# Optimization experiments

Hardware: AMD Instinct MI355X
Metric: run time of the kernel (lower is better)

## Reference

```python
import jax, jax.numpy as jnp
import numpy as np

B, N, D_IN, D_H, D_OUT = 32, 512, 512, 512, 512


def _xavier(key, fan_in, fan_out):
    bound = np.sqrt(6.0 / (fan_in + fan_out))
    return jax.random.uniform(key, (fan_in, fan_out), jnp.float32, -bound, bound)


def setup_inputs() -> dict:
    key = jax.random.key(0)
    ks = jax.random.split(key, 8)
    batch_graph = jax.random.normal(ks[0], (B, N, D_IN), jnp.float32)
    adj = jax.random.uniform(ks[1], (B, N, N), jnp.float32)  # per-graph adjacency blocks
    W0 = _xavier(ks[2], D_IN, D_H)
    b0 = jnp.zeros((D_H,), jnp.float32)
    W1 = _xavier(ks[3], D_H, D_H)
    b1 = jnp.zeros((D_H,), jnp.float32)
    W2 = _xavier(ks[4], D_H, D_OUT)
    b2 = jnp.zeros((D_OUT,), jnp.float32)
    return {"batch_graph": batch_graph, "adj": adj,
            "W0": W0, "b0": b0, "W1": W1, "b1": b1, "W2": W2, "b2": b2}


def _gcn_layer(h, adj, W, b):
    # GraphConvolution: adj @ (h @ W) + b, batched per graph.
    # Equivalent to big_adj @ (big_graph @ W) since big_adj is block-diagonal.
    support = jnp.einsum('bnd,de->bne', h, W)
    return jnp.einsum('bnm,bme->bne', adj, support) + b


def reference(batch_graph, adj, W0, b0, W1, b1, W2, b2):
    # dropout is identity at inference time
    h = jax.nn.relu(_gcn_layer(batch_graph, adj, W0, b0))
    h = jax.nn.relu(_gcn_layer(h, adj, W1, b1))
    h = _gcn_layer(h, adj, W2, b2)  # no activation on final layer
    return h  # [B, N, D_OUT] == torch.stack(big_graph.split(N))
```

## Files before the change

kernel.cpp:

```cpp
#include <hip/hip_runtime.h>
#include <stdint.h>

typedef __bf16 bf16x8 __attribute__((ext_vector_type(8)));
typedef float f32x4 __attribute__((ext_vector_type(4)));
typedef unsigned short u16x4 __attribute__((ext_vector_type(4)));

static __device__ __forceinline__ unsigned short f2bf(float f) {
    union { float f; unsigned u; } v; v.f = f;
    unsigned r = (v.u + 0x7FFFu + ((v.u >> 16) & 1u)) >> 16;
    return (unsigned short)r;
}

__global__ void prep_kernel(const float* __restrict__ X,
                            const float* __restrict__ adj,
                            const float* __restrict__ W0,
                            const float* __restrict__ W1,
                            const float* __restrict__ W2,
                            unsigned short* __restrict__ bufH,
                            unsigned short* __restrict__ adjB,
                            unsigned short* __restrict__ Wt) {
    const int bid = blockIdx.x;
    const int t = threadIdx.x;
    if (bid < 16384) {
        const float* src = (bid < 8192) ? X : adj;
        unsigned short* dst = (bid < 8192) ? bufH : adjB;
        const int i = (bid & 8191) * 256 + t;
        f32x4 v = ((const f32x4*)src)[i];
        u16x4 o;
        o.x = f2bf(v.x); o.y = f2bf(v.y); o.z = f2bf(v.z); o.w = f2bf(v.w);
        ((u16x4*)dst)[i] = o;
    } else {
        const int wb = bid - 16384;
        const int z = wb >> 8;
        const int tile = wb & 255;
        const float* W = (z == 0) ? W0 : (z == 1) ? W1 : W2;
        unsigned short* out = Wt + (size_t)z * (512 * 512);
        __shared__ float tileS[32][33];
        const int bx = (tile & 15) * 32, by = (tile >> 4) * 32;
        const int tx = t & 31, ty = t >> 5;
        #pragma unroll
        for (int r = 0; r < 32; r += 8)
            tileS[ty + r][tx] = W[(size_t)(by + ty + r) * 512 + (bx + tx)];
        __syncthreads();
        #pragma unroll
        for (int r = 0; r < 32; r += 8)
            out[(size_t)(bx + ty + r) * 512 + (by + tx)] = f2bf(tileS[tx][ty + r]);
    }
}

template<int LDA, int LDB, int LDO, bool BIAS, bool RELU, typename OT>
__global__ __launch_bounds__(256, 2)
void gemm_abT_ct(const unsigned short* __restrict__ A,
                 const unsigned short* __restrict__ B,
                 OT* __restrict__ out, const float* __restrict__ bias,
                 long batchA, long batchB, long batchO) {
    __shared__ unsigned short As[2][128 * 64];
    __shared__ unsigned short Bs[2][128 * 64];

    const int tid  = threadIdx.x;
    const int lane = tid & 63;
    const int wave = tid >> 6;
    const int quad = lane >> 4;
    const int l16  = lane & 15;
    const int wm   = wave & 1;
    const int wn   = wave >> 1;

    const int m0 = blockIdx.x * 128;
    const int n0 = blockIdx.y * 128;
    A   += (size_t)blockIdx.z * batchA;
    B   += (size_t)blockIdx.z * batchB;
    out += (size_t)blockIdx.z * batchO;

    const int trow8 = tid >> 3;
    const int tpos8 = (tid & 7) ^ (trow8 & 7);
    const unsigned short* aG = A + (size_t)(m0 + trow8) * LDA + tpos8 * 8;
    const unsigned short* bG = B + (size_t)(n0 + trow8) * LDB + tpos8 * 8;

    f32x4 acc[4][4];
    #pragma unroll
    for (int i = 0; i < 4; ++i)
        #pragma unroll
        for (int j = 0; j < 4; ++j) {
            f32x4 z = {0.f, 0.f, 0.f, 0.f};
            acc[i][j] = z;
        }

#define STAGE(buf, ko)                                                         \
    do {                                                                       \
        char* aL = (char*)As[buf] + tid * 16;                                  \
        char* bL = (char*)Bs[buf] + tid * 16;                                  \
        _Pragma("unroll")                                                      \
        for (int r = 0; r < 4; ++r)                                            \
            __builtin_amdgcn_global_load_lds(                                  \
                (__attribute__((address_space(1))) void*)(uintptr_t)(aG + (size_t)(r * 32) * LDA + (ko)), \
                (__attribute__((address_space(3))) void*)(aL + r * 4096), 16, 0, 0); \
        _Pragma("unroll")                                                      \
        for (int r = 0; r < 4; ++r)                                            \
            __builtin_amdgcn_global_load_lds(                                  \
                (__attribute__((address_space(1))) void*)(uintptr_t)(bG + (size_t)(r * 32) * LDB + (ko)), \
                (__attribute__((address_space(3))) void*)(bL + r * 4096), 16, 0, 0); \
    } while (0)

#define COMPUTE(buf)                                                           \
    do {                                                                       \
        _Pragma("unroll")                                                      \
        for (int ks = 0; ks < 2; ++ks) {                                       \
            bf16x8 af[4], bfr[4];                                              \
            _Pragma("unroll")                                                  \
            for (int i = 0; i < 4; ++i) {                                      \
                const int row = wm * 64 + i * 16 + l16;                        \
                const int idx = row * 8 + ((ks * 4 + quad) ^ (row & 7));       \
                af[i] = *(const bf16x8*)((const char*)As[buf] + idx * 16);     \
            }                                                                  \
            _Pragma("unroll")                                                  \
            for (int j = 0; j < 4; ++j) {                                      \
                const int row = wn * 64 + j * 16 + l16;                        \
                const int idx = row * 8 + ((ks * 4 + quad) ^ (row & 7));       \
                bfr[j] = *(const bf16x8*)((const char*)Bs[buf] + idx * 16);    \
            }                                                                  \
            _Pragma("unroll")                                                  \
            for (int i = 0; i < 4; ++i)                                        \
                _Pragma("unroll")                                              \
                for (int j = 0; j < 4; ++j)                                    \
                    acc[i][j] = __builtin_amdgcn_mfma_f32_16x16x32_bf16(af[i], bfr[j], acc[i][j], 0, 0, 0); \
        }                                                                      \
    } while (0)

    STAGE(0, 0);
    __syncthreads();

    #pragma unroll 1
    for (int kp = 0; kp < 4; ++kp) {
        STAGE(1, kp * 128 + 64);
        COMPUTE(0);
        __syncthreads();
        if (kp < 3) STAGE(0, kp * 128 + 128);
        COMPUTE(1);
        __syncthreads();
    }
#undef STAGE
#undef COMPUTE

    #pragma unroll
    for (int i = 0; i < 4; ++i) {
        const int mb = m0 + wm * 64 + i * 16 + quad * 4;
        f32x4 bb = {0.f, 0.f, 0.f, 0.f};
        if constexpr (BIAS) bb = *(const f32x4*)(bias + mb);
        #pragma unroll
        for (int j = 0; j < 4; ++j) {
            const int n = n0 + wn * 64 + j * 16 + l16;
            f32x4 v = acc[i][j];
            if constexpr (BIAS) v += bb;
            if constexpr (RELU) {
                v.x = v.x > 0.f ? v.x : 0.f;
                v.y = v.y > 0.f ? v.y : 0.f;
                v.z = v.z > 0.f ? v.z : 0.f;
                v.w = v.w > 0.f ? v.w : 0.f;
            }
            if constexpr (sizeof(OT) == 4) {
                *(f32x4*)((float*)out + (size_t)n * LDO + mb) = v;
            } else {
                u16x4 o;
                o.x = f2bf(v.x); o.y = f2bf(v.y); o.z = f2bf(v.z); o.w = f2bf(v.w);
                *(u16x4*)((unsigned short*)out + (size_t)n * LDO + mb) = o;
            }
        }
    }
}

extern "C" void kernel_launch(void* const* d_in, const int* in_sizes, int n_in,
                              void* d_out, int out_size, void* d_ws, size_t ws_size,
                              hipStream_t stream) {
    (void)in_sizes; (void)n_in; (void)out_size; (void)ws_size;
    const float* X   = (const float*)d_in[0];
    const float* adj = (const float*)d_in[1];
    const float* W0  = (const float*)d_in[2];
    const float* b0  = (const float*)d_in[3];
    const float* W1  = (const float*)d_in[4];
    const float* b1  = (const float*)d_in[5];
    const float* W2  = (const float*)d_in[6];
    const float* b2  = (const float*)d_in[7];
    float* out = (float*)d_out;

    char* ws = (char*)d_ws;
    const size_t SZ = 16777216;
    unsigned short* adjB = (unsigned short*)(ws);
    unsigned short* bufH = (unsigned short*)(ws + SZ);
    unsigned short* tmpT = (unsigned short*)(ws + 2 * SZ);
    unsigned short* Wt   = (unsigned short*)(ws + 3 * SZ);
    const unsigned short* W0t = Wt;
    const unsigned short* W1t = Wt + 262144;
    const unsigned short* W2t = Wt + 2 * 262144;

    prep_kernel<<<16384 + 768, 256, 0, stream>>>(X, adj, W0, W1, W2, bufH, adjB, Wt);

    const long BATCH = 512L * 512L;

    gemm_abT_ct<512, 512, 16384, false, false, unsigned short>
        <<<dim3(128, 4, 1), 256, 0, stream>>>(bufH, W0t, tmpT, nullptr, 0, 0, 0);
    gemm_abT_ct<16384, 512, 512, true, true, unsigned short>
        <<<dim3(4, 4, 32), 256, 0, stream>>>(tmpT, adjB, bufH, b0, 512, BATCH, BATCH);
    gemm_abT_ct<512, 512, 16384, false, false, unsigned short>
        <<<dim3(128, 4, 1), 256, 0, stream>>>(bufH, W1t, tmpT, nullptr, 0, 0, 0);
    gemm_abT_ct<16384, 512, 512, true, true, unsigned short>
        <<<dim3(4, 4, 32), 256, 0, stream>>>(tmpT, adjB, bufH, b1, 512, BATCH, BATCH);
    gemm_abT_ct<512, 512, 16384, false, false, unsigned short>
        <<<dim3(128, 4, 1), 256, 0, stream>>>(bufH, W2t, tmpT, nullptr, 0, 0, 0);
    gemm_abT_ct<16384, 512, 512, true, false, float>
        <<<dim3(4, 4, 32), 256, 0, stream>>>(tmpT, adjB, out, b2, 512, BATCH, BATCH);
}
```

Baseline: 229.2 us.

## Fuse six GEMM launches into one persistent kernel with grid barriers

Replaces the six separate GEMM launches with a single persistent 512-block kernel that runs each stage and separates them with atomic-counter grid-wide barriers. The counters are reset inside the prep kernel. The GEMM main loop is also reworked to keep two K-stages in flight, using explicit vmcnt waits, raw s_barrier and s_setprio around the MFMA blocks. The aim is to remove launch gaps and tail effects between dependent stages. In exchange it depends on all 512 blocks being co-resident (2 per CU) to avoid deadlock, and it adds spin-wait overhead.

```diff
diff --git a/kernel.cpp b/kernel.cpp
--- a/kernel.cpp
+++ b/kernel.cpp
@@ -18,10 +18,12 @@
                             const float* __restrict__ W2,
                             unsigned short* __restrict__ bufH,
                             unsigned short* __restrict__ adjB,
-                            unsigned short* __restrict__ Wt) {
+                            unsigned short* __restrict__ Wt,
+                            unsigned* __restrict__ syncc) {
     const int bid = blockIdx.x;
     const int t = threadIdx.x;
     if (bid < 16384) {
+        if (bid == 0 && t < 8) syncc[t] = 0u;
         const float* src = (bid < 8192) ? X : adj;
         unsigned short* dst = (bid < 8192) ? bufH : adjB;
         const int i = (bid & 8191) * 256 + t;
@@ -48,15 +50,25 @@
     }
 }
 
+static __device__ __forceinline__ void gsync(unsigned* __restrict__ cnt) {
+    __syncthreads();
+    __threadfence();
+    if (threadIdx.x == 0) {
+        atomicAdd(cnt, 1u);
+        while (__hip_atomic_load(cnt, __ATOMIC_RELAXED, __HIP_MEMORY_SCOPE_AGENT) < 512u)
+            __builtin_amdgcn_s_sleep(2);
+    }
+    __syncthreads();
+    __threadfence();
+}
+
 template<int LDA, int LDB, int LDO, bool BIAS, bool RELU, typename OT>
-__global__ __launch_bounds__(256, 2)
-void gemm_abT_ct(const unsigned short* __restrict__ A,
-                 const unsigned short* __restrict__ B,
-                 OT* __restrict__ out, const float* __restrict__ bias,
-                 long batchA, long batchB, long batchO) {
-    __shared__ unsigned short As[2][128 * 64];
-    __shared__ unsigned short Bs[2][128 * 64];
-
+static __device__ __forceinline__
+void gemm_stage(const unsigned short* __restrict__ A,
+                const unsigned short* __restrict__ B,
+                OT* __restrict__ out, const float* __restrict__ bias,
+                int m0, int n0,
+                unsigned short (*As)[128 * 64], unsigned short (*Bs)[128 * 64]) {
     const int tid  = threadIdx.x;
     const int lane = tid & 63;
     const int wave = tid >> 6;
@@ -65,12 +77,6 @@
     const int wm   = wave & 1;
     const int wn   = wave >> 1;
 
-    const int m0 = blockIdx.x * 128;
-    const int n0 = blockIdx.y * 128;
-    A   += (size_t)blockIdx.z * batchA;
-    B   += (size_t)blockIdx.z * batchB;
-    out += (size_t)blockIdx.z * batchO;
-
     const int trow8 = tid >> 3;
     const int tpos8 = (tid & 7) ^ (trow8 & 7);
     const unsigned short* aG = A + (size_t)(m0 + trow8) * LDA + tpos8 * 8;
@@ -87,8 +93,8 @@
 
 #define STAGE(buf, ko)                                                         \
     do {                                                                       \
-        char* aL = (char*)As[buf] + tid * 16;                                  \
-        char* bL = (char*)Bs[buf] + tid * 16;                                  \
+        char* aL = (char*)(As[buf]) + tid * 16;                                \
+        char* bL = (char*)(Bs[buf]) + tid * 16;                                \
         _Pragma("unroll")                                                      \
         for (int r = 0; r < 4; ++r)                                            \
             __builtin_amdgcn_global_load_lds(                                  \
@@ -110,13 +116,13 @@
             for (int i = 0; i < 4; ++i) {                                      \
                 const int row = wm * 64 + i * 16 + l16;                        \
                 const int idx = row * 8 + ((ks * 4 + quad) ^ (row & 7));       \
-                af[i] = *(const bf16x8*)((const char*)As[buf] + idx * 16);     \
+                af[i] = *(const bf16x8*)((const char*)(As[buf]) + idx * 16);   \
             }                                                                  \
             _Pragma("unroll")                                                  \
             for (int j = 0; j < 4; ++j) {                                      \
                 const int row = wn * 64 + j * 16 + l16;                        \
                 const int idx = row * 8 + ((ks * 4 + quad) ^ (row & 7));       \
-                bfr[j] = *(const bf16x8*)((const char*)Bs[buf] + idx * 16);    \
+                bfr[j] = *(const bf16x8*)((const char*)(Bs[buf]) + idx * 16);  \
             }                                                                  \
             _Pragma("unroll")                                                  \
             for (int i = 0; i < 4; ++i)                                        \
@@ -127,16 +133,30 @@
     } while (0)
 
     STAGE(0, 0);
-    __syncthreads();
+    STAGE(1, 64);
 
     #pragma unroll 1
     for (int kp = 0; kp < 4; ++kp) {
-        STAGE(1, kp * 128 + 64);
+        const int ko = kp * 128;
+        asm volatile("s_waitcnt vmcnt(8)" ::: "memory");
+        __builtin_amdgcn_s_barrier();
+        __builtin_amdgcn_s_setprio(1);
         COMPUTE(0);
-        __syncthreads();
-        if (kp < 3) STAGE(0, kp * 128 + 128);
+        __builtin_amdgcn_s_setprio(0);
+        asm volatile("s_waitcnt lgkmcnt(0)" ::: "memory");
+        __builtin_amdgcn_sched_barrier(0);
+        __builtin_amdgcn_s_barrier();
+        if (kp < 3) STAGE(0, ko + 128);
+        if (kp < 3) asm volatile("s_waitcnt vmcnt(8)" ::: "memory");
+        else        asm volatile("s_waitcnt vmcnt(0)" ::: "memory");
+        __builtin_amdgcn_s_barrier();
+        __builtin_amdgcn_s_setprio(1);
         COMPUTE(1);
-        __syncthreads();
+        __builtin_amdgcn_s_setprio(0);
+        asm volatile("s_waitcnt lgkmcnt(0)" ::: "memory");
+        __builtin_amdgcn_sched_barrier(0);
+        __builtin_amdgcn_s_barrier();
+        if (kp < 3) STAGE(1, ko + 192);
     }
 #undef STAGE
 #undef COMPUTE
@@ -168,6 +188,41 @@
     }
 }
 
+__global__ __launch_bounds__(256, 2)
+void gcn_fused(unsigned short* __restrict__ bufH,
+               unsigned short* __restrict__ tmpT,
+               const unsigned short* __restrict__ adjB,
+               const unsigned short* __restrict__ Wt,
+               const float* __restrict__ b0, const float* __restrict__ b1,
+               const float* __restrict__ b2, float* __restrict__ out,
+               unsigned* __restrict__ syncc) {
+    __shared__ unsigned short As[2][128 * 64];
+    __shared__ unsigned short Bs[2][128 * 64];
+
+    const int bid = blockIdx.x;
+    const int tm0 = (bid & 127) * 128;
+    const int tn0 = (bid >> 7) * 128;
+    const int am0 = (bid & 3) * 128;
+    const int an0 = ((bid >> 2) & 3) * 128;
+    const long z  = bid >> 4;
+    const unsigned short* Az = tmpT + z * 512;
+    const unsigned short* Bz = adjB + z * 262144;
+    unsigned short* Hz = bufH + z * 262144;
+    float* Oz = out + z * 262144;
+
+    gemm_stage<512, 512, 16384, false, false, unsigned short>(bufH, Wt, tmpT, nullptr, tm0, tn0, As, Bs);
+    gsync(syncc + 0);
+    gemm_stage<16384, 512, 512, true, true, unsigned short>(Az, Bz, Hz, b0, am0, an0, As, Bs);
+    gsync(syncc + 1);
+    gemm_stage<512, 512, 16384, false, false, unsigned short>(bufH, Wt + 262144, tmpT, nullptr, tm0, tn0, As, Bs);
+    gsync(syncc + 2);
+    gemm_stage<16384, 512, 512, true, true, unsigned short>(Az, Bz, Hz, b1, am0, an0, As, Bs);
+    gsync(syncc + 3);
+    gemm_stage<512, 512, 16384, false, false, unsigned short>(bufH, Wt + 2 * 262144, tmpT, nullptr, tm0, tn0, As, Bs);
+    gsync(syncc + 4);
+    gemm_stage<16384, 512, 512, true, false, float>(Az, Bz, Oz, b2, am0, an0, As, Bs);
+}
+
 extern "C" void kernel_launch(void* const* d_in, const int* in_sizes, int n_in,
                               void* d_out, int out_size, void* d_ws, size_t ws_size,
                               hipStream_t stream) {
@@ -188,24 +243,8 @@
     unsigned short* bufH = (unsigned short*)(ws + SZ);
     unsigned short* tmpT = (unsigned short*)(ws + 2 * SZ);
     unsigned short* Wt   = (unsigned short*)(ws + 3 * SZ);
-    const unsigned short* W0t = Wt;
-    const unsigned short* W1t = Wt + 262144;
-    const unsigned short* W2t = Wt + 2 * 262144;
-
-    prep_kernel<<<16384 + 768, 256, 0, stream>>>(X, adj, W0, W1, W2, bufH, adjB, Wt);
-
-    const long BATCH = 512L * 512L;
-
-    gemm_abT_ct<512, 512, 16384, false, false, unsigned short>
-        <<<dim3(128, 4, 1), 256, 0, stream>>>(bufH, W0t, tmpT, nullptr, 0, 0, 0);
-    gemm_abT_ct<16384, 512, 512, true, true, unsigned short>
-        <<<dim3(4, 4, 32), 256, 0, stream>>>(tmpT, adjB, bufH, b0, 512, BATCH, BATCH);
-    gemm_abT_ct<512, 512, 16384, false, false, unsigned short>
-        <<<dim3(128, 4, 1), 256, 0, stream>>>(bufH, W1t, tmpT, nullptr, 0, 0, 0);
-    gemm_abT_ct<16384, 512, 512, true, true, unsigned short>
-        <<<dim3(4, 4, 32), 256, 0, stream>>>(tmpT, adjB, bufH, b1, 512, BATCH, BATCH);
-    gemm_abT_ct<512, 512, 16384, false, false, unsigned short>
-        <<<dim3(128, 4, 1), 256, 0, stream>>>(bufH, W2t, tmpT, nullptr, 0, 0, 0);
-    gemm_abT_ct<16384, 512, 512, true, false, float>
-        <<<dim3(4, 4, 32), 256, 0, stream>>>(tmpT, adjB, out, b2, 512, BATCH, BATCH);
-}
+    unsigned*       sync = (unsigned*)(ws + 3 * SZ + 4 * 1024 * 1024);
+
+    prep_kernel<<<16384 + 768, 256, 0, stream>>>(X, adj, W0, W1, W2, bufH, adjB, Wt, sync);
+    gcn_fused<<<512, 256, 0, stream>>>(bufH, tmpT, adjB, Wt, b0, b1, b2, out, sync);
+}
```

After: 781.9 us. 3.41x slower.

## Keep two K-stages in flight with fine-grained vmcnt waits and wave priority

Applied to the files above, without the earlier changes.

Restructures the double-buffered GEMM main loop so both LDS buffers are prefetched up front, and each compute phase waits only for its own buffer's loads using partial s_waitcnt vmcnt counts instead of a full __syncthreads drain. Raw s_barrier and sched_barrier replace syncthreads, and s_setprio raises wave priority around the MFMA blocks. The aim is deeper overlap of global-to-LDS copies with MFMA work. The hand-tuned waitcnt values depend on the exact number of outstanding loads, so any mismatch would be a correctness risk.

```diff
diff --git a/kernel.cpp b/kernel.cpp
--- a/kernel.cpp
+++ b/kernel.cpp
@@ -87,8 +87,8 @@
 
 #define STAGE(buf, ko)                                                         \
     do {                                                                       \
-        char* aL = (char*)As[buf] + tid * 16;                                  \
-        char* bL = (char*)Bs[buf] + tid * 16;                                  \
+        char* aL = (char*)(As[buf]) + tid * 16;                                \
+        char* bL = (char*)(Bs[buf]) + tid * 16;                                \
         _Pragma("unroll")                                                      \
         for (int r = 0; r < 4; ++r)                                            \
             __builtin_amdgcn_global_load_lds(                                  \
@@ -110,13 +110,13 @@
             for (int i = 0; i < 4; ++i) {                                      \
                 const int row = wm * 64 + i * 16 + l16;                        \
                 const int idx = row * 8 + ((ks * 4 + quad) ^ (row & 7));       \
-                af[i] = *(const bf16x8*)((const char*)As[buf] + idx * 16);     \
+                af[i] = *(const bf16x8*)((const char*)(As[buf]) + idx * 16);   \
             }                                                                  \
             _Pragma("unroll")                                                  \
             for (int j = 0; j < 4; ++j) {                                      \
                 const int row = wn * 64 + j * 16 + l16;                        \
                 const int idx = row * 8 + ((ks * 4 + quad) ^ (row & 7));       \
-                bfr[j] = *(const bf16x8*)((const char*)Bs[buf] + idx * 16);    \
+                bfr[j] = *(const bf16x8*)((const char*)(Bs[buf]) + idx * 16);  \
             }                                                                  \
             _Pragma("unroll")                                                  \
             for (int i = 0; i < 4; ++i)                                        \
@@ -127,16 +127,30 @@
     } while (0)
 
     STAGE(0, 0);
-    __syncthreads();
+    STAGE(1, 64);
 
     #pragma unroll 1
     for (int kp = 0; kp < 4; ++kp) {
-        STAGE(1, kp * 128 + 64);
+        const int ko = kp * 128;
+        asm volatile("s_waitcnt vmcnt(8)" ::: "memory");
+        __builtin_amdgcn_s_barrier();
+        __builtin_amdgcn_s_setprio(1);
         COMPUTE(0);
-        __syncthreads();
-        if (kp < 3) STAGE(0, kp * 128 + 128);
+        __builtin_amdgcn_s_setprio(0);
+        asm volatile("s_waitcnt lgkmcnt(0)" ::: "memory");
+        __builtin_amdgcn_sched_barrier(0);
+        __builtin_amdgcn_s_barrier();
+        if (kp < 3) STAGE(0, ko + 128);
+        if (kp < 3) asm volatile("s_waitcnt vmcnt(8)" ::: "memory");
+        else        asm volatile("s_waitcnt vmcnt(0)" ::: "memory");
+        __builtin_amdgcn_s_barrier();
+        __builtin_amdgcn_s_setprio(1);
         COMPUTE(1);
-        __syncthreads();
+        __builtin_amdgcn_s_setprio(0);
+        asm volatile("s_waitcnt lgkmcnt(0)" ::: "memory");
+        __builtin_amdgcn_sched_barrier(0);
+        __builtin_amdgcn_s_barrier();
+        if (kp < 3) STAGE(1, ko + 192);
     }
 #undef STAGE
 #undef COMPUTE
```

Result: no change. 228.5 us (-0.3%).
